# Optimization experiments

Hardware: AMD Instinct MI355X
Metric: run time of the kernel (lower is better)

## Reference

```python
import jax, jax.numpy as jnp
import numpy as np

NEG_SLOPE = 0.01  # torch LeakyReLU default
MIN_FREQ = 1.0
MAX_FREQ = 10.0
W = 100
N_HIDDEN = 100
N_OBS = 64

def _leaky(x):
    return jnp.where(x >= 0, x, NEG_SLOPE * x)

def setup_inputs() -> dict:
    key = jax.random.key(0)
    ks = jax.random.split(key, 7)
    # kaiming_uniform-ish init scales (exact init doesn't matter for correctness baseline)
    def unif(k, shape, fan_in):
        bound = np.sqrt(6.0 / fan_in)
        return jax.random.uniform(k, shape, jnp.float32, -bound, bound)
    x = jax.random.normal(ks[0], (65536, N_OBS), jnp.float32)
    W_in = unif(ks[1], (N_OBS, W), N_OBS)
    b_in = jnp.zeros((W,), jnp.float32)
    Ws = unif(ks[2], (N_HIDDEN, W, W), W)
    bs = jnp.zeros((N_HIDDEN, W), jnp.float32)
    W_out = unif(ks[3], (W, 1), W)
    b_out = jnp.zeros((1,), jnp.float32)
    return {"x": x, "W_in": W_in, "b_in": b_in, "Ws": Ws, "bs": bs,
            "W_out": W_out, "b_out": b_out}

def reference(x, W_in, b_in, Ws, bs, W_out, b_out):
    h = _leaky(x @ W_in + b_in)                       # [B, 100]
    def layer(h, wb):
        w, b = wb
        return _leaky(h @ w + b), None
    h, _ = jax.lax.scan(layer, h, (Ws, bs))           # 100 hidden layers
    a = h @ W_out + b_out                             # [B, 1]
    a = jnp.tanh(a)
    return (a + 1.0) / 2.0 * (MAX_FREQ - MIN_FREQ) + MIN_FREQ
```

## Files before the change

kernel.cpp:

```cpp
#include <hip/hip_runtime.h>
#include <cmath>

#define NLAYERS 100
#define DIN     64
#define WDIM    100
#define NTT     4
#define ROWS    32
#define WAVES   4
#define BROWS   (WAVES * ROWS)
#define KS      7
#define KSL     3
#define KST     (KS - KSL)
#define FRAGSL  (KSL * NTT)
#define FPW     (FRAGSL / WAVES)

typedef _Float16 half8  __attribute__((ext_vector_type(8)));
typedef _Float16 half2v __attribute__((ext_vector_type(2)));
typedef __fp16   fp16x2 __attribute__((ext_vector_type(2)));
typedef float    f32x4  __attribute__((ext_vector_type(4)));
typedef float    f32x16 __attribute__((ext_vector_type(16)));
typedef unsigned uint4v __attribute__((ext_vector_type(4)));

#define WSH_LAYER_HALVES (KS * NTT * 64 * 8)
#define WSH_HALVES       (NLAYERS * WSH_LAYER_HALVES)
#define W0_HALVES        (4 * NTT * 64 * 8)
#define BPAD_FLOATS      128
#define OFF_BPAD_B       ((WSH_HALVES + W0_HALVES) * 2)
#define OFF_WOUT_B       (OFF_BPAD_B + BPAD_FLOATS * 4)
#define WOUT_FLOATS      128

__global__ __launch_bounds__(256)
void actor_prep(const float* __restrict__ Win, const float* __restrict__ bin,
                const float* __restrict__ Ws,  const float* __restrict__ bs,
                const float* __restrict__ Wout,
                _Float16* __restrict__ wsh, _Float16* __restrict__ w0sh,
                float* __restrict__ bpad, float* __restrict__ woutp) {
    __shared__ float tile[16 * 128];
    const int bid = blockIdx.x, tid = threadIdx.x;
    if (bid < NLAYERS * KS) {
        const int l = bid / KS, ks = bid % KS;
#pragma unroll
        for (int e = 0; e < 8; ++e) {
            int idx = tid + 256 * e;
            int kk = idx >> 7, nn = idx & 127;
            int k = ks * 16 + kk;
            float v = 0.f;
            if (k < WDIM && nn < WDIM)        v = Ws[(l * WDIM + k) * WDIM + nn];
            else if (k == WDIM && nn < WDIM)  v = bs[l * WDIM + nn];
            else if (k == WDIM && nn == WDIM) v = 1.0f;
            tile[idx] = v;
        }
        __syncthreads();
        const int lane = tid & 63, nt = tid >> 6;
        const int g = lane >> 5, n = nt * 32 + (lane & 31);
        half8 o;
#pragma unroll
        for (int j = 0; j < 8; ++j) o[j] = (_Float16)tile[(g * 8 + j) * 128 + n];
        *(half8*)(wsh + (((l * KS + ks) * NTT + nt) << 9) + lane * 8) = o;
        return;
    }
    int b2 = bid - NLAYERS * KS;
    if (b2 < 4) {
        const int ks = b2;
#pragma unroll
        for (int e = 0; e < 8; ++e) {
            int idx = tid + 256 * e;
            int kk = idx >> 7, nn = idx & 127;
            int k = ks * 16 + kk;
            tile[idx] = (nn < WDIM) ? Win[k * WDIM + nn] : 0.f;
        }
        __syncthreads();
        const int lane = tid & 63, nt = tid >> 6;
        const int g = lane >> 5, n = nt * 32 + (lane & 31);
        half8 o;
#pragma unroll
        for (int j = 0; j < 8; ++j) o[j] = (_Float16)tile[(g * 8 + j) * 128 + n];
        *(half8*)(w0sh + ((ks * NTT + nt) << 9) + lane * 8) = o;
        return;
    }
    if (tid < BPAD_FLOATS) {
        bpad[tid] = (tid < WDIM) ? bin[tid] : (tid == WDIM ? 1.0f : 0.f);
    } else {
        int t = tid - BPAD_FLOATS;
        if (t < WOUT_FLOATS) woutp[t] = (t < WDIM) ? Wout[t] : 0.f;
    }
}

__device__ __forceinline__ void stage16(const _Float16* __restrict__ g,
                                        _Float16* l) {
    __builtin_amdgcn_global_load_lds(
        (const __attribute__((address_space(1))) unsigned*)g,
        (__attribute__((address_space(3))) unsigned*)l, 16, 0, 0);
}

__device__ __forceinline__ void split8(const float* __restrict__ p, half8& hi, half8& lo) {
    f32x4 u0 = *(const f32x4*)p;
    f32x4 u1 = *(const f32x4*)(p + 4);
    float v[8] = {u0[0], u0[1], u0[2], u0[3], u1[0], u1[1], u1[2], u1[3]};
#pragma unroll
    for (int e = 0; e < 8; e += 2) {
        fp16x2 h = __builtin_amdgcn_cvt_pkrtz(v[e], v[e + 1]);
        float r0 = v[e]     - (float)h[0];
        float r1 = v[e + 1] - (float)h[1];
        fp16x2 l = __builtin_amdgcn_cvt_pkrtz(r0, r1);
        hi[e] = (_Float16)h[0]; hi[e + 1] = (_Float16)h[1];
        lo[e] = (_Float16)l[0]; lo[e + 1] = (_Float16)l[1];
    }
}

__device__ __forceinline__ unsigned pack2(float a, float b) {
    half2v p; p[0] = (_Float16)a; p[1] = (_Float16)b;
    const half2v slope = {(_Float16)0.01f, (_Float16)0.01f};
    p = __builtin_elementwise_max(p, p * slope);
    return __builtin_bit_cast(unsigned, p);
}

__device__ __forceinline__ void pack_bh(const f32x16 (&acc)[NTT], half8 (&bh)[KS]) {
#pragma unroll
    for (int ks = 0; ks < KS; ++ks) {
        const int r0 = 8 * (ks & 1);
        const f32x16 a = acc[ks >> 1];
        unsigned lo0 = pack2(a[r0 + 0], a[r0 + 1]);
        unsigned lo1 = pack2(a[r0 + 2], a[r0 + 3]);
        unsigned hi0 = pack2(a[r0 + 4], a[r0 + 5]);
        unsigned hi1 = pack2(a[r0 + 6], a[r0 + 7]);
        asm volatile("v_permlane32_swap_b32 %0, %1" : "+v"(lo0), "+v"(hi0));
        asm volatile("v_permlane32_swap_b32 %0, %1" : "+v"(lo1), "+v"(hi1));
        uint4v u = {lo0, lo1, hi0, hi1};
        bh[ks] = __builtin_bit_cast(half8, u);
    }
}

static __device__ const f32x16 kZero16 = {0,0,0,0, 0,0,0,0, 0,0,0,0, 0,0,0,0};

__global__ __launch_bounds__(256, 2)
void actor_main(const float* __restrict__ x,
                const _Float16* __restrict__ wsh,
                const _Float16* __restrict__ w0sh,
                const float* __restrict__ bpad,
                const float* __restrict__ woutp,
                const float* __restrict__ bout,
                float* __restrict__ out) {
    __shared__ __align__(16) _Float16 wlds[2 * FRAGSL * 512];
    const int tid  = threadIdx.x;
    const int lane = tid & 63;
    const int wid  = tid >> 6;
    const int g = lane >> 5, b31 = lane & 31;
    const int rowbase = blockIdx.x * BROWS + wid * ROWS;

    f32x16 acc[NTT];
    half8 bh[KS];
    half8 wbl[KSL][NTT];
    half8 wbg[KST][NTT];

#pragma unroll
    for (int f = 0; f < FPW; ++f) {
        const int fr = wid * FPW + f;
        stage16(wsh + fr * 512 + lane * 8, wlds + fr * 512);
    }

    {
        half8 w0[4][NTT];
#pragma unroll
        for (int ks = 0; ks < 4; ++ks)
#pragma unroll
            for (int nt = 0; nt < NTT; ++nt)
                w0[ks][nt] = *(const half8*)(w0sh + (ks * NTT + nt) * 512 + lane * 8);
#pragma unroll
        for (int nt = 0; nt < NTT; ++nt)
#pragma unroll
            for (int qd = 0; qd < 4; ++qd) {
                f32x4 tq = *(const f32x4*)(bpad + nt * 32 + 8 * qd + 4 * g);
#pragma unroll
                for (int r = 0; r < 4; ++r) acc[nt][4 * qd + r] = tq[r];
            }
        const float* xr = x + (rowbase + b31) * DIN;
#pragma unroll
        for (int ks = 0; ks < 4; ++ks) {
            half8 xhi, xlo;
            split8(xr + ks * 16 + g * 8, xhi, xlo);
#pragma unroll
            for (int nt = 0; nt < NTT; ++nt) {
                acc[nt] = __builtin_amdgcn_mfma_f32_32x32x16_f16(w0[ks][nt], xhi, acc[nt], 0, 0, 0);
                acc[nt] = __builtin_amdgcn_mfma_f32_32x32x16_f16(w0[ks][nt], xlo, acc[nt], 0, 0, 0);
            }
        }
    }
    pack_bh(acc, bh);
    __syncthreads();

#pragma unroll 1
    for (int l = 0; l < NLAYERS; ++l) {
        const _Float16* rb = wlds + (l & 1) * (FRAGSL * 512);
        _Float16* sb = (_Float16*)wlds + ((l + 1) & 1) * (FRAGSL * 512);
        const _Float16* wg = wsh + l * WSH_LAYER_HALVES;
        const int ln = (l + 1 < NLAYERS) ? l + 1 : NLAYERS - 1;
        const _Float16* wn = wsh + ln * WSH_LAYER_HALVES;

#pragma unroll
        for (int ks = 0; ks < KSL; ++ks)
#pragma unroll
            for (int nt = 0; nt < NTT; ++nt)
                wbl[ks][nt] = *(const half8*)(rb + (ks * NTT + nt) * 512 + lane * 8);
#pragma unroll
        for (int ks = 0; ks < KST; ++ks)
#pragma unroll
            for (int nt = 0; nt < NTT; ++nt)
                wbg[ks][nt] = *(const half8*)(wg + ((KSL + ks) * NTT + nt) * 512 + lane * 8);
#pragma unroll
        for (int f = 0; f < FPW; ++f) {
            const int fr = wid * FPW + f;
            stage16(wn + fr * 512 + lane * 8, sb + fr * 512);
        }
#pragma unroll
        for (int ks = 0; ks < KS; ++ks) {
#pragma unroll
            for (int nt = 0; nt < NTT; ++nt) {
                const half8 wfrag = (ks < KSL) ? wbl[ks][nt] : wbg[ks - KSL][nt];
                acc[nt] = __builtin_amdgcn_mfma_f32_32x32x16_f16(
                    wfrag, bh[ks], (ks == 0 ? kZero16 : acc[nt]), 0, 0, 0);
            }
        }
        if (l < NLAYERS - 1)
            pack_bh(acc, bh);
        __syncthreads();
    }

    float s = 0.f;
#pragma unroll
    for (int nt = 0; nt < NTT; ++nt)
#pragma unroll
        for (int qd = 0; qd < 4; ++qd) {
            f32x4 w4 = *(const f32x4*)(woutp + nt * 32 + 8 * qd + 4 * g);
#pragma unroll
            for (int r = 0; r < 4; ++r) {
                float a = acc[nt][4 * qd + r];
                float v = fmaxf(a, 0.01f * a);
                s += v * w4[r];
            }
        }
    s += __shfl_xor(s, 32);
    if (lane < 32) {
        float tot = s + bout[0];
        out[rowbase + b31] = tanhf(tot) * 4.5f + 5.5f;
    }
}

extern "C" void kernel_launch(void* const* d_in, const int* in_sizes, int n_in,
                              void* d_out, int out_size, void* d_ws, size_t ws_size,
                              hipStream_t stream) {
    const float* x    = (const float*)d_in[0];
    const float* Win  = (const float*)d_in[1];
    const float* bin  = (const float*)d_in[2];
    const float* Ws   = (const float*)d_in[3];
    const float* bs   = (const float*)d_in[4];
    const float* Wout = (const float*)d_in[5];
    const float* bout = (const float*)d_in[6];
    float* out = (float*)d_out;

    char* ws = (char*)d_ws;
    _Float16* wsh  = (_Float16*)ws;
    _Float16* w0sh = wsh + WSH_HALVES;
    float* bpad  = (float*)(ws + OFF_BPAD_B);
    float* woutp = (float*)(ws + OFF_WOUT_B);

    hipLaunchKernelGGL(actor_prep, dim3(NLAYERS * KS + 4 + 1), dim3(256), 0, stream,
                       Win, bin, Ws, bs, Wout, wsh, w0sh, bpad, woutp);

    const int nrows = in_sizes[0] / DIN;
    hipLaunchKernelGGL(actor_main, dim3(nrows / BROWS), dim3(WAVES * 64), 0, stream,
                       x, wsh, w0sh, bpad, woutp, bout, out);
}
```

Measured before the change: 300.7 us.

## Prefetch next layer's register-held weights one layer ahead with double-buffered registers

Splits per-layer weight fragments so four k-slices go through LDS and three are loaded straight into registers, then prefetches the next layer's register fragments during the current layer using two ping-pong register sets. Inline asm global loads and sched_barriers keep the compiler from sinking or merging the prefetch, and the layer loop is unrolled by two so the buffers swap statically. This hides global load latency behind the MFMA chain, at the cost of more VGPRs and more LDS per block, which may limit occupancy at two blocks per CU.

```diff
diff --git a/kernel.cpp b/kernel.cpp
--- a/kernel.cpp
+++ b/kernel.cpp
@@ -9,7 +9,7 @@
 #define WAVES   4
 #define BROWS   (WAVES * ROWS)
 #define KS      7
-#define KSL     3
+#define KSL     4
 #define KST     (KS - KSL)
 #define FRAGSL  (KSL * NTT)
 #define FPW     (FRAGSL / WAVES)
@@ -91,6 +91,18 @@
     __builtin_amdgcn_global_load_lds(
         (const __attribute__((address_space(1))) unsigned*)g,
         (__attribute__((address_space(3))) unsigned*)l, 16, 0, 0);
+}
+
+__device__ __forceinline__ void tcp_load(uint4v (&w)[KST][NTT],
+                                         const _Float16* __restrict__ base, int lane) {
+#pragma unroll
+    for (int ks = 0; ks < KST; ++ks) {
+        const _Float16* bp = base + (KSL + ks) * NTT * 512 + lane * 8;
+        asm volatile("global_load_dwordx4 %0, %1, off"             : "=v"(w[ks][0]) : "v"(bp));
+        asm volatile("global_load_dwordx4 %0, %1, off offset:1024" : "=v"(w[ks][1]) : "v"(bp));
+        asm volatile("global_load_dwordx4 %0, %1, off offset:2048" : "=v"(w[ks][2]) : "v"(bp));
+        asm volatile("global_load_dwordx4 %0, %1, off offset:3072" : "=v"(w[ks][3]) : "v"(bp));
+    }
 }
 
 __device__ __forceinline__ void split8(const float* __restrict__ p, half8& hi, half8& lo) {
@@ -132,6 +144,36 @@
 }
 
 static __device__ const f32x16 kZero16 = {0,0,0,0, 0,0,0,0, 0,0,0,0, 0,0,0,0};
+
+__device__ __forceinline__ void hidden_layer(
+    f32x16 (&acc)[NTT], half8 (&bh)[KS],
+    const _Float16* rb, _Float16* sb, const _Float16* __restrict__ wnext,
+    uint4v (&wbgC)[KST][NTT], uint4v (&wbgN)[KST][NTT],
+    int wid, int lane, bool dopack) {
+#pragma unroll
+    for (int f = 0; f < FPW; ++f) {
+        const int fr = wid * FPW + f;
+        stage16(wnext + fr * 512 + lane * 8, sb + fr * 512);
+    }
+    tcp_load(wbgN, wnext, lane);
+#pragma unroll
+    for (int ks = 0; ks < KSL; ++ks)
+#pragma unroll
+        for (int nt = 0; nt < NTT; ++nt) {
+            half8 wfrag = *(const half8*)(rb + (ks * NTT + nt) * 512 + lane * 8);
+            acc[nt] = __builtin_amdgcn_mfma_f32_32x32x16_f16(
+                wfrag, bh[ks], (ks == 0 ? kZero16 : acc[nt]), 0, 0, 0);
+        }
+#pragma unroll
+    for (int ks = KSL; ks < KS; ++ks)
+#pragma unroll
+        for (int nt = 0; nt < NTT; ++nt)
+            acc[nt] = __builtin_amdgcn_mfma_f32_32x32x16_f16(
+                __builtin_bit_cast(half8, wbgC[ks - KSL][nt]), bh[ks], acc[nt], 0, 0, 0);
+    if (dopack) pack_bh(acc, bh);
+    __syncthreads();
+    __builtin_amdgcn_sched_barrier(0);
+}
 
 __global__ __launch_bounds__(256, 2)
 void actor_main(const float* __restrict__ x,
@@ -150,14 +192,15 @@
 
     f32x16 acc[NTT];
     half8 bh[KS];
-    half8 wbl[KSL][NTT];
-    half8 wbg[KST][NTT];
+    uint4v wbgA[KST][NTT];
+    uint4v wbgB[KST][NTT];
 
 #pragma unroll
     for (int f = 0; f < FPW; ++f) {
         const int fr = wid * FPW + f;
         stage16(wsh + fr * 512 + lane * 8, wlds + fr * 512);
     }
+    tcp_load(wbgA, wsh, lane);
 
     {
         half8 w0[4][NTT];
@@ -188,42 +231,18 @@
     }
     pack_bh(acc, bh);
     __syncthreads();
-
+    __builtin_amdgcn_sched_barrier(0);
+
+    _Float16* buf0 = wlds;
+    _Float16* buf1 = wlds + FRAGSL * 512;
 #pragma unroll 1
-    for (int l = 0; l < NLAYERS; ++l) {
-        const _Float16* rb = wlds + (l & 1) * (FRAGSL * 512);
-        _Float16* sb = (_Float16*)wlds + ((l + 1) & 1) * (FRAGSL * 512);
-        const _Float16* wg = wsh + l * WSH_LAYER_HALVES;
-        const int ln = (l + 1 < NLAYERS) ? l + 1 : NLAYERS - 1;
-        const _Float16* wn = wsh + ln * WSH_LAYER_HALVES;
-
-#pragma unroll
-        for (int ks = 0; ks < KSL; ++ks)
-#pragma unroll
-            for (int nt = 0; nt < NTT; ++nt)
-                wbl[ks][nt] = *(const half8*)(rb + (ks * NTT + nt) * 512 + lane * 8);
-#pragma unroll
-        for (int ks = 0; ks < KST; ++ks)
-#pragma unroll
-            for (int nt = 0; nt < NTT; ++nt)
-                wbg[ks][nt] = *(const half8*)(wg + ((KSL + ks) * NTT + nt) * 512 + lane * 8);
-#pragma unroll
-        for (int f = 0; f < FPW; ++f) {
-            const int fr = wid * FPW + f;
-            stage16(wn + fr * 512 + lane * 8, sb + fr * 512);
-        }
-#pragma unroll
-        for (int ks = 0; ks < KS; ++ks) {
-#pragma unroll
-            for (int nt = 0; nt < NTT; ++nt) {
-                const half8 wfrag = (ks < KSL) ? wbl[ks][nt] : wbg[ks - KSL][nt];
-                acc[nt] = __builtin_amdgcn_mfma_f32_32x32x16_f16(
-                    wfrag, bh[ks], (ks == 0 ? kZero16 : acc[nt]), 0, 0, 0);
-            }
-        }
-        if (l < NLAYERS - 1)
-            pack_bh(acc, bh);
-        __syncthreads();
+    for (int l = 0; l < NLAYERS; l += 2) {
+        const int l1 = (l + 1 < NLAYERS) ? l + 1 : NLAYERS - 1;
+        const int l2 = (l + 2 < NLAYERS) ? l + 2 : NLAYERS - 1;
+        hidden_layer(acc, bh, buf0, buf1, wsh + l1 * WSH_LAYER_HALVES,
+                     wbgA, wbgB, wid, lane, true);
+        hidden_layer(acc, bh, buf1, buf0, wsh + l2 * WSH_LAYER_HALVES,
+                     wbgB, wbgA, wid, lane, l + 1 < NLAYERS - 1);
     }
 
     float s = 0.f;
```

Result: faster. 270.6 us (-10.0%).
